# Kernel tuning notes

Measured on AMD Instinct MI355X. Metric: run time of the kernel, lower is better.

The kernel has to match this reference:

```python
import jax, jax.numpy as jnp
import numpy as np

V, E, H, L, B, S = 32000, 256, 512, 2, 128, 512


def _lstm_step(x, h, c, w_ih, w_hh, b_ih, b_hh):
    # PyTorch gate order: i, f, g, o
    gates = x @ w_ih.T + b_ih + h @ w_hh.T + b_hh
    i, f, g, o = jnp.split(gates, 4, axis=-1)
    c2 = jax.nn.sigmoid(f) * c + jax.nn.sigmoid(i) * jnp.tanh(g)
    h2 = jax.nn.sigmoid(o) * jnp.tanh(c2)
    return h2, c2


def setup_inputs() -> dict:
    key = jax.random.key(0)
    ks = jax.random.split(key, 16)
    s = 0.05
    d = {}
    d["dec_input"] = jax.random.randint(ks[0], (B,), 0, V)
    d["hidden"] = jax.random.normal(ks[1], (L, B, H), jnp.float32)
    d["cell"] = jax.random.normal(ks[2], (L, B, H), jnp.float32)
    d["encoder_outputs"] = jax.random.normal(ks[3], (S, B, H), jnp.float32)
    d["emb"] = jax.random.normal(ks[4], (V, E), jnp.float32) * s
    d["attn_w"] = jax.random.normal(ks[5], (1, 2 * H), jnp.float32) * s
    d["attn_b"] = jnp.zeros((1,), jnp.float32)
    d["w_ih0"] = jax.random.normal(ks[6], (4 * H, E + H), jnp.float32) * s
    d["w_hh0"] = jax.random.normal(ks[7], (4 * H, H), jnp.float32) * s
    d["b_ih0"] = jnp.zeros((4 * H,), jnp.float32)
    d["b_hh0"] = jnp.zeros((4 * H,), jnp.float32)
    d["w_ih1"] = jax.random.normal(ks[8], (4 * H, H), jnp.float32) * s
    d["w_hh1"] = jax.random.normal(ks[9], (4 * H, H), jnp.float32) * s
    d["b_ih1"] = jnp.zeros((4 * H,), jnp.float32)
    d["b_hh1"] = jnp.zeros((4 * H,), jnp.float32)
    d["fc_w"] = jax.random.normal(ks[10], (V, H), jnp.float32) * s
    d["fc_b"] = jnp.zeros((V,), jnp.float32)
    return d


def reference(dec_input, hidden, cell, encoder_outputs, emb, attn_w, attn_b,
              w_ih0, w_hh0, b_ih0, b_hh0, w_ih1, w_hh1, b_ih1, b_hh1,
              fc_w, fc_b):
    # embedded: [B, E]  (dropout p=0 -> identity)
    embedded = emb[dec_input]
    # Bahdanau-style additive scoring using FIRST-layer hidden (as in source)
    h0 = hidden[0]                                   # [B, H]
    w_enc, w_hid = attn_w[0, :H], attn_w[0, H:]      # split linear over concat
    # logits[b,s] = enc[s,b]@w_enc + h0[b]@w_hid + b
    logits = jnp.einsum('sbh,h->bs', encoder_outputs, w_enc) \
        + (h0 @ w_hid)[:, None] + attn_b[0]          # [B, S]
    alpha = jax.nn.softmax(logits, axis=1)           # softmax over src positions
    # context = sum_s alpha[b,s] * enc[s,b,:]  (avoids repeat_interleave blowup)
    context = jnp.einsum('bs,sbh->bh', alpha, encoder_outputs)  # [B, H]
    x = jnp.concatenate([context, embedded], axis=1)            # [B, H+E]
    # single-timestep 2-layer LSTM
    h_0, c_0 = _lstm_step(x, hidden[0], cell[0], w_ih0, w_hh0, b_ih0, b_hh0)
    h_1, c_1 = _lstm_step(h_0, hidden[1], cell[1], w_ih1, w_hh1, b_ih1, b_hh1)
    new_hidden = jnp.stack([h_0, h_1])
    new_cell = jnp.stack([c_0, c_1])
    prediction = h_1 @ fc_w.T + fc_b                 # [B, V]
    return prediction, new_hidden, new_cell
```

## Files before the change

kernel.cpp:

```cpp
#include <hip/hip_runtime.h>
#include <hip/hip_bf16.h>
#include <math.h>

constexpr int NV = 32000;
constexpr int NE = 256;
constexpr int NH = 512;
constexpr int NB = 128;
constexpr int NS = 512;
constexpr int NX = NH + NE;
constexpr int NSC = 8;

typedef __attribute__((ext_vector_type(8))) short short8;
typedef __attribute__((ext_vector_type(4))) short short4v;
typedef __attribute__((ext_vector_type(4))) float f32x4;

constexpr size_t OFF_PCTX  = 0;
constexpr size_t OFF_PML   = OFF_PCTX  + (size_t)NB*NSC*NH;
constexpr size_t OFF_XBF   = OFF_PML   + (size_t)NB*NSC*2;
constexpr size_t OFF_H0NBF = OFF_XBF   + 49152;
constexpr size_t OFF_H1NBF = OFF_H0NBF + 32768;

constexpr size_t OUT_HID  = (size_t)NB * NV;
constexpr size_t OUT_CELL = OUT_HID + 2ull * NB * NH;

__device__ inline float sigf(float x) { return 1.0f / (1.0f + expf(-x)); }
__device__ inline short bf16s(float x) {
  __hip_bfloat16 h = __float2bfloat16(x);
  return *reinterpret_cast<short*>(&h);
}

__global__ __launch_bounds__(256) void attn_partial_k(
    const float* __restrict__ enc, const float* __restrict__ attn_w,
    float* __restrict__ pctx, float* __restrict__ pml) {
  const int sc = blockIdx.x, b = blockIdx.y;
  const int wv = threadIdx.x >> 6, lane = threadIdx.x & 63;
  const f32x4 wa = *reinterpret_cast<const f32x4*>(attn_w + lane * 4);
  const f32x4 wb = *reinterpret_cast<const f32x4*>(attn_w + 256 + lane * 4);
  float m0 = -INFINITY, l0 = 0.f, m1 = -INFINITY, l1 = 0.f;
  f32x4 a00 = {}, a01 = {}, a10 = {}, a11 = {};
  const float* base = enc + ((size_t)(sc * 64 + wv) * NB + b) * NH;
  for (int i = 0; i < 8; ++i) {
    const float* r0 = base + (size_t)(i * 4) * NB * NH;
    const float* r1 = base + (size_t)((i + 8) * 4) * NB * NH;
    f32x4 e00 = *reinterpret_cast<const f32x4*>(r0 + lane * 4);
    f32x4 e01 = *reinterpret_cast<const f32x4*>(r0 + 256 + lane * 4);
    f32x4 e10 = *reinterpret_cast<const f32x4*>(r1 + lane * 4);
    f32x4 e11 = *reinterpret_cast<const f32x4*>(r1 + 256 + lane * 4);
    float d0 = e00.x * wa.x + e00.y * wa.y + e00.z * wa.z + e00.w * wa.w
             + e01.x * wb.x + e01.y * wb.y + e01.z * wb.z + e01.w * wb.w;
    float d1 = e10.x * wa.x + e10.y * wa.y + e10.z * wa.z + e10.w * wa.w
             + e11.x * wb.x + e11.y * wb.y + e11.z * wb.z + e11.w * wb.w;
#pragma unroll
    for (int off = 32; off; off >>= 1) {
      d0 += __shfl_xor(d0, off);
      d1 += __shfl_xor(d1, off);
    }
    float mn0 = fmaxf(m0, d0), mn1 = fmaxf(m1, d1);
    float s0 = expf(m0 - mn0), s1 = expf(m1 - mn1);
    float p0 = expf(d0 - mn0), p1 = expf(d1 - mn1);
    l0 = l0 * s0 + p0;         l1 = l1 * s1 + p1;
    a00 = a00 * s0 + p0 * e00; a01 = a01 * s0 + p0 * e01;
    a10 = a10 * s1 + p1 * e10; a11 = a11 * s1 + p1 * e11;
    m0 = mn0; m1 = mn1;
  }
  const float Mw = fmaxf(m0, m1);
  const float c0 = expf(m0 - Mw), c1 = expf(m1 - Mw);
  const float lw = l0 * c0 + l1 * c1;
  const f32x4 accA = a00 * c0 + a10 * c1;
  const f32x4 accB = a01 * c0 + a11 * c1;
  __shared__ float sm[4], sl[4], sacc[4][NH];
  if (lane == 0) { sm[wv] = Mw; sl[wv] = lw; }
  *reinterpret_cast<f32x4*>(&sacc[wv][lane * 4]) = accA;
  *reinterpret_cast<f32x4*>(&sacc[wv][256 + lane * 4]) = accB;
  __syncthreads();
  const float M = fmaxf(fmaxf(sm[0], sm[1]), fmaxf(sm[2], sm[3]));
  const float e0 = expf(sm[0] - M), e1 = expf(sm[1] - M),
              e2 = expf(sm[2] - M), e3 = expf(sm[3] - M);
  const int t = threadIdx.x;
  float* outc = pctx + ((size_t)b * NSC + sc) * NH;
#pragma unroll
  for (int q = 0; q < 2; ++q) {
    int h = q * 256 + t;
    outc[h] = sacc[0][h] * e0 + sacc[1][h] * e1 + sacc[2][h] * e2 + sacc[3][h] * e3;
  }
  if (t == 0) {
    pml[((size_t)b * NSC + sc) * 2 + 0] = M;
    pml[((size_t)b * NSC + sc) * 2 + 1] = sl[0] * e0 + sl[1] * e1 + sl[2] * e2 + sl[3] * e3;
  }
}

__global__ __launch_bounds__(256) void attn_finish_k(
    const float* __restrict__ pctx, const float* __restrict__ pml,
    const float* __restrict__ emb, const int* __restrict__ dec,
    __hip_bfloat16* __restrict__ xbf) {
  const int b = blockIdx.x, t = threadIdx.x;
  float ms[NSC];
  float M = -INFINITY;
#pragma unroll
  for (int sc = 0; sc < NSC; ++sc) {
    ms[sc] = pml[((size_t)b * NSC + sc) * 2 + 0];
    M = fmaxf(M, ms[sc]);
  }
  float L = 0.f, es[NSC];
#pragma unroll
  for (int sc = 0; sc < NSC; ++sc) {
    es[sc] = expf(ms[sc] - M);
    L += pml[((size_t)b * NSC + sc) * 2 + 1] * es[sc];
  }
  const float invL = 1.f / L;
#pragma unroll
  for (int q = 0; q < 2; ++q) {
    int h = q * 256 + t;
    float v = 0.f;
#pragma unroll
    for (int sc = 0; sc < NSC; ++sc)
      v += pctx[((size_t)b * NSC + sc) * NH + h] * es[sc];
    xbf[(size_t)b * NX + h] = __float2bfloat16(v * invL);
  }
  xbf[(size_t)b * NX + NH + t] = __float2bfloat16(emb[(size_t)dec[b] * NE + t]);
}

__global__ __launch_bounds__(512) void fused_lstm_k(
    const __hip_bfloat16* __restrict__ Abf, int strideA, int K0,
    const float* __restrict__ Wih,
    const float* __restrict__ hf32, const float* __restrict__ Whh,
    const float* __restrict__ b_ih, const float* __restrict__ b_hh,
    const float* __restrict__ c_in,
    float* __restrict__ h_out, float* __restrict__ c_out,
    __hip_bfloat16* __restrict__ hbf_out) {
  const int wid = threadIdx.x >> 6, lane = threadIdx.x & 63;
  const int gate = wid & 3, part = wid >> 2;
  const int l15 = lane & 15, lhi = lane >> 4;
  const int mtile = blockIdx.x >> 5, h16 = blockIdx.x & 31;
  const int n = gate * NH + h16 * 16 + l15;
  f32x4 acc = {};
  if (part == 0) {
    const float* wrow = Wih + (size_t)n * K0 + lhi * 8;
    const __hip_bfloat16* arow = Abf + (size_t)(mtile * 16 + l15) * strideA + lhi * 8;
#pragma unroll 4
    for (int k0 = 0; k0 < K0; k0 += 32) {
      f32x4 w0 = *reinterpret_cast<const f32x4*>(wrow + k0);
      f32x4 w1 = *reinterpret_cast<const f32x4*>(wrow + k0 + 4);
      short8 bfrag;
      bfrag[0] = bf16s(w0.x); bfrag[1] = bf16s(w0.y);
      bfrag[2] = bf16s(w0.z); bfrag[3] = bf16s(w0.w);
      bfrag[4] = bf16s(w1.x); bfrag[5] = bf16s(w1.y);
      bfrag[6] = bf16s(w1.z); bfrag[7] = bf16s(w1.w);
      short8 afrag = *reinterpret_cast<const short8*>(arow + k0);
      acc = __builtin_amdgcn_mfma_f32_16x16x32_bf16(afrag, bfrag, acc, 0, 0, 0);
    }
  } else {
    const float* wrow = Whh + (size_t)n * NH + lhi * 8;
    const float* arow = hf32 + (size_t)(mtile * 16 + l15) * NH + lhi * 8;
#pragma unroll 4
    for (int k0 = 0; k0 < NH; k0 += 32) {
      f32x4 w0 = *reinterpret_cast<const f32x4*>(wrow + k0);
      f32x4 w1 = *reinterpret_cast<const f32x4*>(wrow + k0 + 4);
      f32x4 a0 = *reinterpret_cast<const f32x4*>(arow + k0);
      f32x4 a1 = *reinterpret_cast<const f32x4*>(arow + k0 + 4);
      short8 bfrag, afrag;
      bfrag[0] = bf16s(w0.x); bfrag[1] = bf16s(w0.y);
      bfrag[2] = bf16s(w0.z); bfrag[3] = bf16s(w0.w);
      bfrag[4] = bf16s(w1.x); bfrag[5] = bf16s(w1.y);
      bfrag[6] = bf16s(w1.z); bfrag[7] = bf16s(w1.w);
      afrag[0] = bf16s(a0.x); afrag[1] = bf16s(a0.y);
      afrag[2] = bf16s(a0.z); afrag[3] = bf16s(a0.w);
      afrag[4] = bf16s(a1.x); afrag[5] = bf16s(a1.y);
      afrag[6] = bf16s(a1.z); afrag[7] = bf16s(a1.w);
      acc = __builtin_amdgcn_mfma_f32_16x16x32_bf16(afrag, bfrag, acc, 0, 0, 0);
    }
  }
  __shared__ float sg[8][16][17];
#pragma unroll
  for (int r = 0; r < 4; ++r) sg[wid][lhi * 4 + r][l15] = acc[r];
  __syncthreads();
  const int t = threadIdx.x;
  if (t < 256) {
    const int row = t >> 4, col = t & 15;
    const int b = mtile * 16 + row, h = h16 * 16 + col;
    float ig = sg[0][row][col] + sg[4][row][col] + b_ih[0 * NH + h] + b_hh[0 * NH + h];
    float fg = sg[1][row][col] + sg[5][row][col] + b_ih[1 * NH + h] + b_hh[1 * NH + h];
    float gg = sg[2][row][col] + sg[6][row][col] + b_ih[2 * NH + h] + b_hh[2 * NH + h];
    float og = sg[3][row][col] + sg[7][row][col] + b_ih[3 * NH + h] + b_hh[3 * NH + h];
    float c = c_in[(size_t)b * NH + h];
    float c2 = sigf(fg) * c + sigf(ig) * tanhf(gg);
    float h2 = sigf(og) * tanhf(c2);
    c_out[(size_t)b * NH + h] = c2;
    h_out[(size_t)b * NH + h] = h2;
    hbf_out[(size_t)b * NH + h] = __float2bfloat16(h2);
  }
}

constexpr int FC_PANELS = 8;
constexpr int FC_BLOCKS = NV / (16 * FC_PANELS);
constexpr int SLAB = 520;

__global__ __launch_bounds__(256, 1) void gemm_fc_pipe_k(
    const __hip_bfloat16* __restrict__ Abf, const float* __restrict__ W,
    const float* __restrict__ bias, float* __restrict__ out) {
  __shared__ short wlds[2][16 * SLAB];
  const int tid = threadIdx.x, wv = tid >> 6, lane = tid & 63;
  const int l15 = lane & 15, lhi = lane >> 4;
  const int nbase = blockIdx.x * (16 * FC_PANELS);

  int soff[8];
#pragma unroll
  for (int i = 0; i < 8; ++i) {
    const int o = i * 1024 + tid * 4;
    const int n = o >> 9, kk = o & 511;
    soff[i] = (kk >> 5) * SLAB + n * 32 + (kk & 31);
  }

  short8 af[2][16];
#pragma unroll
  for (int m = 0; m < 2; ++m) {
    const __hip_bfloat16* ar = Abf + (size_t)(wv * 32 + m * 16 + l15) * NH + lhi * 8;
#pragma unroll
    for (int ks = 0; ks < 16; ++ks)
      af[m][ks] = *reinterpret_cast<const short8*>(ar + ks * 32);
  }

  f32x4 wr[8];
  {
    const float* panel = W + (size_t)nbase * NH;
#pragma unroll
    for (int i = 0; i < 8; ++i)
      wr[i] = *reinterpret_cast<const f32x4*>(panel + i * 1024 + tid * 4);
    short* wb0 = wlds[0];
#pragma unroll
    for (int i = 0; i < 8; ++i) {
      short4v cv;
      cv[0] = bf16s(wr[i].x); cv[1] = bf16s(wr[i].y);
      cv[2] = bf16s(wr[i].z); cv[3] = bf16s(wr[i].w);
      *reinterpret_cast<short4v*>(wb0 + soff[i]) = cv;
    }
  }
  __syncthreads();

  f32x4 s0 = {}, s1 = {};
  int sn0 = -1;
  for (int p = 0; p < FC_PANELS; ++p) {
    if (p < FC_PANELS - 1) {
      const float* panel = W + (size_t)(nbase + (p + 1) * 16) * NH;
#pragma unroll
      for (int i = 0; i < 8; ++i)
        wr[i] = *reinterpret_cast<const f32x4*>(panel + i * 1024 + tid * 4);
    }
    if (sn0 >= 0) {
      const float bv = bias[sn0 + l15];
#pragma unroll
      for (int q = 0; q < 4; ++q) {
        out[(size_t)(wv * 32 + 0 * 16 + lhi * 4 + q) * NV + sn0 + l15] = s0[q] + bv;
        out[(size_t)(wv * 32 + 1 * 16 + lhi * 4 + q) * NV + sn0 + l15] = s1[q] + bv;
      }
    }
    {
      const short* wb = wlds[p & 1];
      f32x4 a0 = {}, a1 = {};
#pragma unroll
      for (int ks = 0; ks < 16; ++ks) {
        short8 bf = *reinterpret_cast<const short8*>(wb + ks * SLAB + l15 * 32 + lhi * 8);
        a0 = __builtin_amdgcn_mfma_f32_16x16x32_bf16(af[0][ks], bf, a0, 0, 0, 0);
        a1 = __builtin_amdgcn_mfma_f32_16x16x32_bf16(af[1][ks], bf, a1, 0, 0, 0);
      }
      s0 = a0; s1 = a1; sn0 = nbase + p * 16;
    }
    if (p < FC_PANELS - 1) {
      short* wbn = wlds[(p + 1) & 1];
#pragma unroll
      for (int i = 0; i < 8; ++i) {
        short4v cv;
        cv[0] = bf16s(wr[i].x); cv[1] = bf16s(wr[i].y);
        cv[2] = bf16s(wr[i].z); cv[3] = bf16s(wr[i].w);
        *reinterpret_cast<short4v*>(wbn + soff[i]) = cv;
      }
      __syncthreads();
    }
  }
  {
    const float bv = bias[sn0 + l15];
#pragma unroll
    for (int q = 0; q < 4; ++q) {
      out[(size_t)(wv * 32 + 0 * 16 + lhi * 4 + q) * NV + sn0 + l15] = s0[q] + bv;
      out[(size_t)(wv * 32 + 1 * 16 + lhi * 4 + q) * NV + sn0 + l15] = s1[q] + bv;
    }
  }
}

extern "C" void kernel_launch(void* const* d_in, const int* in_sizes, int n_in,
                              void* d_out, int out_size, void* d_ws, size_t ws_size,
                              hipStream_t stream) {
  const int*   dec    = (const int*)d_in[0];
  const float* hidden = (const float*)d_in[1];
  const float* cell   = (const float*)d_in[2];
  const float* enc    = (const float*)d_in[3];
  const float* emb    = (const float*)d_in[4];
  const float* attn_w = (const float*)d_in[5];
  const float* w_ih0  = (const float*)d_in[7];
  const float* w_hh0  = (const float*)d_in[8];
  const float* b_ih0  = (const float*)d_in[9];
  const float* b_hh0  = (const float*)d_in[10];
  const float* w_ih1  = (const float*)d_in[11];
  const float* w_hh1  = (const float*)d_in[12];
  const float* b_ih1  = (const float*)d_in[13];
  const float* b_hh1  = (const float*)d_in[14];
  const float* fc_w   = (const float*)d_in[15];
  const float* fc_b   = (const float*)d_in[16];
  float* out = (float*)d_out;
  float* ws  = (float*)d_ws;

  float* pctx = ws + OFF_PCTX;
  float* pml  = ws + OFF_PML;
  __hip_bfloat16* xbf   = (__hip_bfloat16*)(ws + OFF_XBF);
  __hip_bfloat16* h0nbf = (__hip_bfloat16*)(ws + OFF_H0NBF);
  __hip_bfloat16* h1nbf = (__hip_bfloat16*)(ws + OFF_H1NBF);

  attn_partial_k<<<dim3(NSC, NB), 256, 0, stream>>>(enc, attn_w, pctx, pml);
  attn_finish_k<<<NB, 256, 0, stream>>>(pctx, pml, emb, dec, xbf);
  fused_lstm_k<<<256, 512, 0, stream>>>(xbf, NX, NX, w_ih0, hidden, w_hh0,
                                        b_ih0, b_hh0, cell,
                                        out + OUT_HID, out + OUT_CELL, h0nbf);
  fused_lstm_k<<<256, 512, 0, stream>>>(h0nbf, NH, NH, w_ih1, hidden + NB * NH, w_hh1,
                                        b_ih1, b_hh1, cell + NB * NH,
                                        out + OUT_HID + (size_t)NB * NH,
                                        out + OUT_CELL + (size_t)NB * NH, h1nbf);
  gemm_fc_pipe_k<<<FC_BLOCKS, 256, 0, stream>>>(h1nbf, fc_w, fc_b, out);
}
```

Measured before the change: 81.67 us.

## Split LSTM into weight-reusing LDS-pipelined GEMM plus pointwise kernel

Replaces the fused LSTM kernel with two kernels. The first is a GEMM in which each block stages a 16-column slab of fp32 weights into LDS as bf16, double-buffered, and reuses it across all 128 batch rows. The second applies the gates pointwise. Previously each block covered only 16 batch rows, so every weight was re-read and re-converted eight times. The hidden state is now converted to bf16 once, inside the attention finish kernel. The cost is two extra launches and a round trip of the gate buffer through global memory, and only 128 blocks per GEMM, which may leave CUs idle.

New measurement: 78.53 us. 1.04x faster.

```diff
diff --git a/kernel.cpp b/kernel.cpp
--- a/kernel.cpp
+++ b/kernel.cpp
@@ -8,6 +8,7 @@
 constexpr int NB = 128;
 constexpr int NS = 512;
 constexpr int NX = NH + NE;
+constexpr int NG = 2048;
 constexpr int NSC = 8;
 
 typedef __attribute__((ext_vector_type(8))) short short8;
@@ -19,6 +20,9 @@
 constexpr size_t OFF_XBF   = OFF_PML   + (size_t)NB*NSC*2;
 constexpr size_t OFF_H0NBF = OFF_XBF   + 49152;
 constexpr size_t OFF_H1NBF = OFF_H0NBF + 32768;
+constexpr size_t OFF_H0BFI = OFF_H1NBF + 32768;
+constexpr size_t OFF_H1BFI = OFF_H0BFI + 32768;
+constexpr size_t OFF_GBUF  = OFF_H1BFI + 32768;
 
 constexpr size_t OUT_HID  = (size_t)NB * NV;
 constexpr size_t OUT_CELL = OUT_HID + 2ull * NB * NH;
@@ -92,7 +96,9 @@
 __global__ __launch_bounds__(256) void attn_finish_k(
     const float* __restrict__ pctx, const float* __restrict__ pml,
     const float* __restrict__ emb, const int* __restrict__ dec,
-    __hip_bfloat16* __restrict__ xbf) {
+    const float* __restrict__ hidden,
+    __hip_bfloat16* __restrict__ xbf,
+    __hip_bfloat16* __restrict__ h0bf, __hip_bfloat16* __restrict__ h1bf) {
   const int b = blockIdx.x, t = threadIdx.x;
   float ms[NSC];
   float M = -INFINITY;
@@ -116,79 +122,106 @@
     for (int sc = 0; sc < NSC; ++sc)
       v += pctx[((size_t)b * NSC + sc) * NH + h] * es[sc];
     xbf[(size_t)b * NX + h] = __float2bfloat16(v * invL);
+    h0bf[(size_t)b * NH + h] = __float2bfloat16(hidden[(size_t)b * NH + h]);
+    h1bf[(size_t)b * NH + h] =
+        __float2bfloat16(hidden[(size_t)(NB * NH) + (size_t)b * NH + h]);
   }
   xbf[(size_t)b * NX + NH + t] = __float2bfloat16(emb[(size_t)dec[b] * NE + t]);
 }
 
-__global__ __launch_bounds__(512) void fused_lstm_k(
-    const __hip_bfloat16* __restrict__ Abf, int strideA, int K0,
-    const float* __restrict__ Wih,
-    const float* __restrict__ hf32, const float* __restrict__ Whh,
-    const float* __restrict__ b_ih, const float* __restrict__ b_hh,
-    const float* __restrict__ c_in,
+constexpr int LSLAB = 520;
+__global__ __launch_bounds__(256, 1) void lstm_gemm_k(
+    const float* __restrict__ Wx, int Kx, const float* __restrict__ Wh,
+    const __hip_bfloat16* __restrict__ Ax, const __hip_bfloat16* __restrict__ Ah,
+    float* __restrict__ gbuf) {
+  __shared__ short wlds[2][8 * LSLAB];
+  const int tid = threadIdx.x, wv = tid >> 6, lane = tid & 63;
+  const int l15 = lane & 15, lhi = lane >> 4;
+  const int n0 = blockIdx.x * 16;
+  const int NCHX = Kx >> 8, NCH = NCHX + 2;
+  const int srow = tid >> 6;
+  const int scol = lane * 4;
+  const int soff0 = (scol >> 5) * LSLAB + (scol & 31);
+
+  f32x4 wr[4];
+#define LSTAGE_LOAD(c)                                                        \
+  {                                                                           \
+    const bool fx = (c) < NCHX;                                               \
+    const float* Ws = fx ? Wx : Wh;                                           \
+    const int Ks = fx ? Kx : NH;                                              \
+    const int cb = fx ? (c) * 256 : ((c) - NCHX) * 256;                       \
+    _Pragma("unroll")                                                         \
+    for (int i = 0; i < 4; ++i)                                               \
+      wr[i] = *reinterpret_cast<const f32x4*>(                                \
+          Ws + (size_t)(n0 + i * 4 + srow) * Ks + cb + scol);                 \
+  }
+#define LSTAGE_WRITE(buf)                                                     \
+  {                                                                           \
+    _Pragma("unroll")                                                         \
+    for (int i = 0; i < 4; ++i) {                                             \
+      short4v cv;                                                             \
+      cv[0] = bf16s(wr[i].x); cv[1] = bf16s(wr[i].y);                         \
+      cv[2] = bf16s(wr[i].z); cv[3] = bf16s(wr[i].w);                         \
+      *reinterpret_cast<short4v*>((buf) + soff0 + (i * 4 + srow) * 32) = cv;  \
+    }                                                                         \
+  }
+
+  LSTAGE_LOAD(0);
+  LSTAGE_WRITE(wlds[0]);
+  __syncthreads();
+
+  f32x4 acc0 = {}, acc1 = {};
+  for (int c = 0; c < NCH; ++c) {
+    if (c + 1 < NCH) LSTAGE_LOAD(c + 1);
+    {
+      const bool fx = c < NCHX;
+      const __hip_bfloat16* As = fx ? Ax : Ah;
+      const int Ks = fx ? Kx : NH;
+      const int cb = fx ? c * 256 : (c - NCHX) * 256;
+      const short* wb = wlds[c & 1];
+      const __hip_bfloat16* ar0 = As + (size_t)(wv * 32 + l15) * Ks + cb + lhi * 8;
+      const __hip_bfloat16* ar1 = ar0 + (size_t)16 * Ks;
+#pragma unroll
+      for (int ks = 0; ks < 8; ++ks) {
+        short8 bf = *reinterpret_cast<const short8*>(wb + ks * LSLAB + l15 * 32 + lhi * 8);
+        short8 a0 = *reinterpret_cast<const short8*>(ar0 + ks * 32);
+        short8 a1 = *reinterpret_cast<const short8*>(ar1 + ks * 32);
+        acc0 = __builtin_amdgcn_mfma_f32_16x16x32_bf16(a0, bf, acc0, 0, 0, 0);
+        acc1 = __builtin_amdgcn_mfma_f32_16x16x32_bf16(a1, bf, acc1, 0, 0, 0);
+      }
+    }
+    if (c + 1 < NCH) {
+      LSTAGE_WRITE(wlds[(c + 1) & 1]);
+      __syncthreads();
+    }
+  }
+#pragma unroll
+  for (int q = 0; q < 4; ++q) {
+    gbuf[(size_t)(wv * 32 + lhi * 4 + q) * NG + n0 + l15] = acc0[q];
+    gbuf[(size_t)(wv * 32 + 16 + lhi * 4 + q) * NG + n0 + l15] = acc1[q];
+  }
+#undef LSTAGE_LOAD
+#undef LSTAGE_WRITE
+}
+
+__global__ __launch_bounds__(256) void lstm_point_k(
+    const float* __restrict__ g, const float* __restrict__ b_ih,
+    const float* __restrict__ b_hh, const float* __restrict__ c_in,
     float* __restrict__ h_out, float* __restrict__ c_out,
     __hip_bfloat16* __restrict__ hbf_out) {
-  const int wid = threadIdx.x >> 6, lane = threadIdx.x & 63;
-  const int gate = wid & 3, part = wid >> 2;
-  const int l15 = lane & 15, lhi = lane >> 4;
-  const int mtile = blockIdx.x >> 5, h16 = blockIdx.x & 31;
-  const int n = gate * NH + h16 * 16 + l15;
-  f32x4 acc = {};
-  if (part == 0) {
-    const float* wrow = Wih + (size_t)n * K0 + lhi * 8;
-    const __hip_bfloat16* arow = Abf + (size_t)(mtile * 16 + l15) * strideA + lhi * 8;
-#pragma unroll 4
-    for (int k0 = 0; k0 < K0; k0 += 32) {
-      f32x4 w0 = *reinterpret_cast<const f32x4*>(wrow + k0);
-      f32x4 w1 = *reinterpret_cast<const f32x4*>(wrow + k0 + 4);
-      short8 bfrag;
-      bfrag[0] = bf16s(w0.x); bfrag[1] = bf16s(w0.y);
-      bfrag[2] = bf16s(w0.z); bfrag[3] = bf16s(w0.w);
-      bfrag[4] = bf16s(w1.x); bfrag[5] = bf16s(w1.y);
-      bfrag[6] = bf16s(w1.z); bfrag[7] = bf16s(w1.w);
-      short8 afrag = *reinterpret_cast<const short8*>(arow + k0);
-      acc = __builtin_amdgcn_mfma_f32_16x16x32_bf16(afrag, bfrag, acc, 0, 0, 0);
-    }
-  } else {
-    const float* wrow = Whh + (size_t)n * NH + lhi * 8;
-    const float* arow = hf32 + (size_t)(mtile * 16 + l15) * NH + lhi * 8;
-#pragma unroll 4
-    for (int k0 = 0; k0 < NH; k0 += 32) {
-      f32x4 w0 = *reinterpret_cast<const f32x4*>(wrow + k0);
-      f32x4 w1 = *reinterpret_cast<const f32x4*>(wrow + k0 + 4);
-      f32x4 a0 = *reinterpret_cast<const f32x4*>(arow + k0);
-      f32x4 a1 = *reinterpret_cast<const f32x4*>(arow + k0 + 4);
-      short8 bfrag, afrag;
-      bfrag[0] = bf16s(w0.x); bfrag[1] = bf16s(w0.y);
-      bfrag[2] = bf16s(w0.z); bfrag[3] = bf16s(w0.w);
-      bfrag[4] = bf16s(w1.x); bfrag[5] = bf16s(w1.y);
-      bfrag[6] = bf16s(w1.z); bfrag[7] = bf16s(w1.w);
-      afrag[0] = bf16s(a0.x); afrag[1] = bf16s(a0.y);
-      afrag[2] = bf16s(a0.z); afrag[3] = bf16s(a0.w);
-      afrag[4] = bf16s(a1.x); afrag[5] = bf16s(a1.y);
-      afrag[6] = bf16s(a1.z); afrag[7] = bf16s(a1.w);
-      acc = __builtin_amdgcn_mfma_f32_16x16x32_bf16(afrag, bfrag, acc, 0, 0, 0);
-    }
-  }
-  __shared__ float sg[8][16][17];
-#pragma unroll
-  for (int r = 0; r < 4; ++r) sg[wid][lhi * 4 + r][l15] = acc[r];
-  __syncthreads();
-  const int t = threadIdx.x;
-  if (t < 256) {
-    const int row = t >> 4, col = t & 15;
-    const int b = mtile * 16 + row, h = h16 * 16 + col;
-    float ig = sg[0][row][col] + sg[4][row][col] + b_ih[0 * NH + h] + b_hh[0 * NH + h];
-    float fg = sg[1][row][col] + sg[5][row][col] + b_ih[1 * NH + h] + b_hh[1 * NH + h];
-    float gg = sg[2][row][col] + sg[6][row][col] + b_ih[2 * NH + h] + b_hh[2 * NH + h];
-    float og = sg[3][row][col] + sg[7][row][col] + b_ih[3 * NH + h] + b_hh[3 * NH + h];
-    float c = c_in[(size_t)b * NH + h];
-    float c2 = sigf(fg) * c + sigf(ig) * tanhf(gg);
-    float h2 = sigf(og) * tanhf(c2);
-    c_out[(size_t)b * NH + h] = c2;
-    h_out[(size_t)b * NH + h] = h2;
-    hbf_out[(size_t)b * NH + h] = __float2bfloat16(h2);
-  }
+  const int idx = blockIdx.x * 256 + threadIdx.x;
+  const int h = idx & 511;
+  const size_t base = (size_t)(idx >> 9) * NG;
+  float ig = g[base + 0 * NH + h] + b_ih[0 * NH + h] + b_hh[0 * NH + h];
+  float fg = g[base + 1 * NH + h] + b_ih[1 * NH + h] + b_hh[1 * NH + h];
+  float gg = g[base + 2 * NH + h] + b_ih[2 * NH + h] + b_hh[2 * NH + h];
+  float og = g[base + 3 * NH + h] + b_ih[3 * NH + h] + b_hh[3 * NH + h];
+  float c = c_in[idx];
+  float c2 = sigf(fg) * c + sigf(ig) * tanhf(gg);
+  float h2 = sigf(og) * tanhf(c2);
+  c_out[idx] = c2;
+  h_out[idx] = h2;
+  hbf_out[idx] = __float2bfloat16(h2);
 }
 
 constexpr int FC_PANELS = 8;
@@ -314,15 +347,22 @@
   __hip_bfloat16* xbf   = (__hip_bfloat16*)(ws + OFF_XBF);
   __hip_bfloat16* h0nbf = (__hip_bfloat16*)(ws + OFF_H0NBF);
   __hip_bfloat16* h1nbf = (__hip_bfloat16*)(ws + OFF_H1NBF);
+  __hip_bfloat16* h0bf  = (__hip_bfloat16*)(ws + OFF_H0BFI);
+  __hip_bfloat16* h1bf  = (__hip_bfloat16*)(ws + OFF_H1BFI);
+  float* gbuf = ws + OFF_GBUF;
 
   attn_partial_k<<<dim3(NSC, NB), 256, 0, stream>>>(enc, attn_w, pctx, pml);
-  attn_finish_k<<<NB, 256, 0, stream>>>(pctx, pml, emb, dec, xbf);
-  fused_lstm_k<<<256, 512, 0, stream>>>(xbf, NX, NX, w_ih0, hidden, w_hh0,
-                                        b_ih0, b_hh0, cell,
-                                        out + OUT_HID, out + OUT_CELL, h0nbf);
-  fused_lstm_k<<<256, 512, 0, stream>>>(h0nbf, NH, NH, w_ih1, hidden + NB * NH, w_hh1,
-                                        b_ih1, b_hh1, cell + NB * NH,
-                                        out + OUT_HID + (size_t)NB * NH,
-                                        out + OUT_CELL + (size_t)NB * NH, h1nbf);
+  attn_finish_k<<<NB, 256, 0, stream>>>(pctx, pml, emb, dec, hidden,
+                                        xbf, h0bf, h1bf);
+  lstm_gemm_k<<<NG / 16, 256, 0, stream>>>(w_ih0, NX, w_hh0, xbf, h0bf, gbuf);
+  lstm_point_k<<<NB * NH / 256, 256, 0, stream>>>(gbuf, b_ih0, b_hh0, cell,
+                                                  out + OUT_HID, out + OUT_CELL,
+                                                  h0nbf);
+  lstm_gemm_k<<<NG / 16, 256, 0, stream>>>(w_ih1, NH, w_hh1, h0nbf, h1bf, gbuf);
+  lstm_point_k<<<NB * NH / 256, 256, 0, stream>>>(gbuf, b_ih1, b_hh1,
+                                                  cell + NB * NH,
+                                                  out + OUT_HID + (size_t)NB * NH,
+                                                  out + OUT_CELL + (size_t)NB * NH,
+                                                  h1nbf);
   gemm_fc_pipe_k<<<FC_BLOCKS, 256, 0, stream>>>(h1nbf, fc_w, fc_b, out);
 }
```
